# Kernel tuning notes

Hardware: AMD Instinct MI355X
Metric: run time of the kernel (lower is better)

## Reference

```python
import jax, jax.numpy as jnp
import numpy as np

AXES = 72        # NUM_OF_IMU_AXES
PARAMS = 12      # NUM_OF_NOISE_PARAMS
MAX_PROP = 600   # max_propogation
LN_EPS = 1e-5    # nn.LayerNorm default eps


def setup_inputs() -> dict:
    key = jax.random.key(0)
    k0, k1 = jax.random.split(key, 2)
    S, D = 4096, 512
    hidden_states = jax.random.normal(k0, (1, S, D), jnp.float32)
    gamma = jnp.ones((D,), jnp.float32)          # LayerNorm weight
    beta = jnp.zeros((D,), jnp.float32)          # LayerNorm bias
    W = jax.random.normal(k1, (D, AXES * PARAMS), jnp.float32) * 0.02  # Linear weight (in,out)
    b = jnp.zeros((AXES * PARAMS,), jnp.float32)
    return {"hidden_states": hidden_states, "gamma": gamma, "beta": beta, "W": W, "b": b}


def reference(hidden_states, gamma, beta, W, b):
    S = hidden_states.shape[1]
    T = min(MAX_PROP, S)  # time_steps_propogate_kinematics (static under jit)

    # LayerNorm over last dim
    x = hidden_states[0]  # (S, D); B == 1 by contract
    mu = jnp.mean(x, axis=-1, keepdims=True)
    var = jnp.mean((x - mu) ** 2, axis=-1, keepdims=True)
    xn = (x - mu) / jnp.sqrt(var + LN_EPS) * gamma + beta

    # Linear -> (seq, params, axes); rearrange 'seq (params axes)' => params outer
    p = (xn @ W + b).reshape(S, PARAMS, AXES)
    sp = jax.nn.softplus

    c, c_th = p[:, 4], p[:, 5]          # (S, A)
    phi, phi_th = p[:, 6], p[:, 7]
    d = sp(p[:, 1]); k = d * d / 4 + sp(p[:, 0])
    d_th = sp(p[:, 3]); k_th = d_th * d_th / 4 + sp(p[:, 2])

    acc_base = p[:, 8].T                # (A, S)
    acc_std = sp(p[:, 9]).T
    gyro_base = p[:, 10].T
    gyro_std = sp(p[:, 11]).T

    t = jnp.arange(T, dtype=jnp.float32)[None, :, None]  # (1, T, 1)

    def osc(cc, dd, kk, ph):
        # damped oscillator value grid, vectorized over all 72 axes: (S, T, A)
        om = jnp.sqrt(4.0 * kk - dd * dd) / 2.0  # = sqrt(softplus)>=0, safe
        return (cc[:, None, :] * jnp.exp(-dd[:, None, :] / 2.0 * t)
                * jnp.sin(t * om[:, None, :] + ph[:, None, :]))

    vals = osc(c, d, k, phi) + osc(c_th, d_th, k_th, phi_th)  # (S, T, A)

    # banded overlap-add: out[s + t] += vals[s, t]; positions >= S are dropped
    pos = (jnp.arange(S)[:, None] + jnp.arange(T)[None, :]).reshape(-1)  # (S*T,)
    vals_flat = vals.reshape(S * T, AXES)
    out = jnp.zeros((S + T, AXES), vals.dtype).at[pos].add(vals_flat)[:S]  # (S, A)
    kinematics = out.T  # (A, S)

    return kinematics, acc_base, acc_std, gyro_base, gyro_std
```

## Files before the change

### kernel.cpp

```cpp
#include <hip/hip_runtime.h>
#include <math.h>

#define S_TOTAL 4096
#define DDIM    512
#define AXES    72
#define NPROJ   864
#define T_PROP  600
#define SA      (S_TOTAL*AXES)
#define LN_EPS  1e-5f
#define AMP_CUT 4e-6f

typedef __attribute__((ext_vector_type(8))) short short8;
typedef __attribute__((ext_vector_type(4))) float f32x4;

__device__ __forceinline__ float softplus_f(float x) {
    return fmaxf(x, 0.f) + log1pf(expf(-fabsf(x)));
}
__device__ __forceinline__ unsigned short bf_hi(float f) {
    return (unsigned short)(__float_as_uint(f) >> 16);
}

__global__ __launch_bounds__(256) void prep_kernel(
        const float* __restrict__ x, const float* __restrict__ gamma,
        const float* __restrict__ beta, const float* __restrict__ W,
        unsigned short* __restrict__ Ahi, unsigned short* __restrict__ Alo,
        unsigned short* __restrict__ WhiT, unsigned short* __restrict__ WloT,
        float* __restrict__ kin) {
    __shared__ float Wt[32][33];
    int tid = threadIdx.x;
    int b = blockIdx.x;
    if (b < 1024) {
        int lane = tid & 63, w = tid >> 6;
        int row = b*4 + w;
        const float4* xr = reinterpret_cast<const float4*>(x + (size_t)row * DDIM);
        float4 xv[2] = { xr[lane], xr[lane + 64] };
        float sum = 0.f, ssq = 0.f;
#pragma unroll
        for (int c = 0; c < 2; ++c) {
            sum += (xv[c].x + xv[c].y) + (xv[c].z + xv[c].w);
            ssq += xv[c].x*xv[c].x + xv[c].y*xv[c].y + xv[c].z*xv[c].z + xv[c].w*xv[c].w;
        }
#pragma unroll
        for (int off = 1; off < 64; off <<= 1) {
            sum += __shfl_xor(sum, off);
            ssq += __shfl_xor(ssq, off);
        }
        float m = sum * (1.f/DDIM);
        float r = rsqrtf(ssq * (1.f/DDIM) - m*m + LN_EPS);
        const float4* gp = reinterpret_cast<const float4*>(gamma);
        const float4* bp = reinterpret_cast<const float4*>(beta);
#pragma unroll
        for (int c = 0; c < 2; ++c) {
            float4 gv = gp[lane + 64*c], bv = bp[lane + 64*c];
            float xn[4] = {(xv[c].x-m)*r*gv.x+bv.x, (xv[c].y-m)*r*gv.y+bv.y,
                           (xv[c].z-m)*r*gv.z+bv.z, (xv[c].w-m)*r*gv.w+bv.w};
            ushort4 h4, l4;
            unsigned short* hp = &h4.x;
            unsigned short* lp = &l4.x;
#pragma unroll
            for (int j = 0; j < 4; ++j) {
                unsigned short hi = bf_hi(xn[j]);
                float fhi = __uint_as_float((unsigned)hi << 16);
                hp[j] = hi;
                lp[j] = bf_hi(xn[j] - fhi);
            }
            size_t o = (size_t)row*DDIM + 256*c + lane*4;
            *reinterpret_cast<ushort4*>(&Ahi[o]) = h4;
            *reinterpret_cast<ushort4*>(&Alo[o]) = l4;
        }
    } else if (b < 1456) {
        int wb = b - 1024;
        int bk = wb / 27, bn = wb - bk*27;
        int tx = tid & 31, ty0 = tid >> 5;
#pragma unroll
        for (int rr = 0; rr < 4; ++rr) {
            int ty = ty0 + rr*8;
            Wt[ty][tx] = W[(size_t)(bk*32 + ty)*NPROJ + bn*32 + tx];
        }
        __syncthreads();
#pragma unroll
        for (int rr = 0; rr < 4; ++rr) {
            int ny = ty0 + rr*8;
            int n = bn*32 + ny;
            int k = bk*32 + tx;
            float f = Wt[tx][ny];
            unsigned short hi = bf_hi(f);
            float fhi = __uint_as_float((unsigned)hi << 16);
            WhiT[(size_t)n*DDIM + k] = hi;
            WloT[(size_t)n*DDIM + k] = bf_hi(f - fhi);
        }
    } else {
        int zb = b - 1456;
        float4 z4 = make_float4(0.f, 0.f, 0.f, 0.f);
        float4* kp = reinterpret_cast<float4*>(kin);
#pragma unroll
        for (int i = 0; i < 8; ++i)
            kp[zb*2048 + i*256 + tid] = z4;
    }
}

__global__ __launch_bounds__(256) void gemm_kernel(
        const unsigned short* __restrict__ Ahi, const unsigned short* __restrict__ Alo,
        const unsigned short* __restrict__ WhiT, const unsigned short* __restrict__ WloT,
        const float* __restrict__ bias,
        float* __restrict__ P, float* __restrict__ out) {
    __shared__ __align__(16) unsigned short ldsArena[2*20480];

    int tid  = threadIdx.x;
    int lane = tid & 63;
    int wv   = tid >> 6;
    int wm   = wv & 1;
    int wn   = wv >> 1;
    int sBase = blockIdx.x * 64;
    int nBase = blockIdx.y * 96;
    int l15 = lane & 15;
    int r7  = l15 & 7;

    int rr = lane >> 3;
    int jj = ((lane & 7) ^ rr) * 8;
    const unsigned short* gp[10];
#pragma unroll
    for (int g = 0; g < 10; ++g) {
        int seg = wv*10 + g;
        const unsigned short* src;
        int row;
        if (seg < 16) {
            int p = seg >> 3, rg = seg & 7;
            row = sBase + rg*8 + rr;
            src = p ? Alo : Ahi;
        } else {
            int s2 = seg - 16;
            int p = (s2 >= 12) ? 1 : 0, rg = s2 - p*12;
            row = nBase + rg*8 + rr;
            src = p ? WloT : WhiT;
        }
        gp[g] = src + (size_t)row*DDIM + jj;
    }

    f32x4 acc[2][3] = {};
    int cur = 0;

#define STAGE(buf, k0) do {                                                   \
        unsigned short* lb = ldsArena + (buf)*20480 + wv*5120;                \
        _Pragma("unroll")                                                     \
        for (int g = 0; g < 10; ++g)                                          \
            __builtin_amdgcn_global_load_lds(                                 \
                (const __attribute__((address_space(1))) void*)(gp[g] + (k0)),\
                (__attribute__((address_space(3))) void*)(lb + g*512),        \
                16, 0, 0);                                                    \
    } while (0)

    STAGE(0, 0);

#pragma unroll 1
    for (int kt = 0; kt < 8; ++kt) {
        __syncthreads();
        if (kt < 7) STAGE(cur ^ 1, (kt+1)*64);

        const char* Bc = (const char*)(ldsArena + cur*20480);
#pragma unroll
        for (int kk = 0; kk < 2; ++kk) {
            int kb = kk*64 + ((lane>>4)<<4);
            short8 xh[2], xl[2], wh[3], wl[3];
#pragma unroll
            for (int mi = 0; mi < 2; ++mi) {
                int row = wm*32 + mi*16 + l15;
                int ad = (row*128 + kb) ^ (r7<<4);
                xh[mi] = *reinterpret_cast<const short8*>(Bc + ad);
                xl[mi] = *reinterpret_cast<const short8*>(Bc + 8192 + ad);
            }
#pragma unroll
            for (int nf = 0; nf < 3; ++nf) {
                int row = wn*48 + nf*16 + l15;
                int ad = (row*128 + kb) ^ (r7<<4);
                wh[nf] = *reinterpret_cast<const short8*>(Bc + 16384 + ad);
                wl[nf] = *reinterpret_cast<const short8*>(Bc + 28672 + ad);
            }
#pragma unroll
            for (int mi = 0; mi < 2; ++mi)
#pragma unroll
                for (int nf = 0; nf < 3; ++nf)
                    acc[mi][nf] = __builtin_amdgcn_mfma_f32_16x16x32_bf16(wh[nf], xh[mi], acc[mi][nf], 0, 0, 0);
#pragma unroll
            for (int mi = 0; mi < 2; ++mi)
#pragma unroll
                for (int nf = 0; nf < 3; ++nf)
                    acc[mi][nf] = __builtin_amdgcn_mfma_f32_16x16x32_bf16(wh[nf], xl[mi], acc[mi][nf], 0, 0, 0);
#pragma unroll
            for (int mi = 0; mi < 2; ++mi)
#pragma unroll
                for (int nf = 0; nf < 3; ++nf)
                    acc[mi][nf] = __builtin_amdgcn_mfma_f32_16x16x32_bf16(wl[nf], xh[mi], acc[mi][nf], 0, 0, 0);
        }
        cur ^= 1;
    }
#undef STAGE

    int sCol = sBase + wm*32 + l15;
    int nRowBase = nBase + wn*48 + ((lane>>4)<<2);
#pragma unroll
    for (int mi = 0; mi < 2; ++mi) {
        int s = sCol + mi*16;
#pragma unroll
        for (int nf = 0; nf < 3; ++nf) {
#pragma unroll
            for (int r = 0; r < 4; ++r) {
                int n = nRowBase + nf*16 + r;
                float val = acc[mi][nf][r] + bias[n];
                int ip = (n * 3641) >> 18;
                int a  = n - ip * 72;
                float res;
                if (ip == 0 || ip == 2)      res = sqrtf(softplus_f(val));
                else if (ip == 1 || ip == 3 || ip == 9 || ip == 11) res = softplus_f(val);
                else                          res = val;
                float* dst = (ip < 8) ? (P + (size_t)ip * SA)
                                      : (out + (size_t)(ip - 7) * SA);
                dst[(size_t)a * S_TOTAL + s] = res;
            }
        }
    }
}

template<int STEPS>
__device__ __forceinline__ void osc_chunk(
        float& v1a, float& v1b, float& v2a, float& v2b,
        float p1, float q1, float p2, float q2,
        float& acc0, float& acc1, int lane, int lane4) {
#pragma unroll
    for (int i = 0; i < STEPS/2; ++i) {
        {
            const int dt = 2*i;
            v1b = fmaf(p1, v1a, -(q1*v1b));
            v2b = fmaf(p2, v2a, -(q2*v2b));
            float v = v1b + v2b;
            if (dt == 0) {
                acc0 += v;
            } else {
                int addr = (lane4 + (((64-dt)&63)<<2)) & 255;
                float vr = __int_as_float(__builtin_amdgcn_ds_bpermute(addr, __float_as_int(v)));
                bool nw = lane >= dt;
                acc0 += nw ? vr : 0.f;
                acc1 += nw ? 0.f : vr;
            }
        }
        {
            const int dt = 2*i + 1;
            v1a = fmaf(p1, v1b, -(q1*v1a));
            v2a = fmaf(p2, v2b, -(q2*v2a));
            float v = v1a + v2a;
            int addr = (lane4 + (((64-dt)&63)<<2)) & 255;
            float vr = __int_as_float(__builtin_amdgcn_ds_bpermute(addr, __float_as_int(v)));
            bool nw = lane >= dt;
            acc0 += nw ? vr : 0.f;
            acc1 += nw ? 0.f : vr;
        }
    }
}

__global__ __launch_bounds__(256) void osc_kernel(const float* __restrict__ P,
                                                  float* __restrict__ kin) {
    int tid  = threadIdx.x;
    int lane = tid & 63;
    int wv   = tid >> 6;
    int lane4 = lane << 2;
    int sBase = blockIdx.x * 64;
    int a  = blockIdx.y * 2 + (wv >> 1);
    int t0 = (wv & 1) * 300;
    float t0f = (float)t0;

    size_t base = (size_t)a * S_TOTAL + sBase + lane;
    float om1 = P[0*(size_t)SA + base], d1 = P[1*(size_t)SA + base];
    float om2 = P[2*(size_t)SA + base], d2 = P[3*(size_t)SA + base];
    float c1  = P[4*(size_t)SA + base], c2  = P[5*(size_t)SA + base];
    float ph1 = P[6*(size_t)SA + base], ph2 = P[7*(size_t)SA + base];

    float dcf1 = __expf(-0.5f*d1);
    float e1   = c1 * __expf(-0.5f*d1*t0f);
    float s0, c0, so, co;
    __sincosf(fmaf(t0f, om1, ph1), &s0, &c0);
    __sincosf(om1, &so, &co);
    float inv1 = __expf(0.5f*d1);
    float p1 = 2.f*dcf1*co, q1 = dcf1*dcf1;
    float v1a = e1*inv1*(s0*co - c0*so);
    float cs2 = fmaf(2.f*co, co, -1.f), sn2 = 2.f*so*co;
    float v1b = e1*inv1*inv1*(s0*cs2 - c0*sn2);
    float amp1 = fabsf(e1);
    float dq1 = q1*q1; dq1*=dq1; dq1*=dq1; dq1*=dq1; dq1*=dq1;
    float dcf2 = __expf(-0.5f*d2);
    float e2   = c2 * __expf(-0.5f*d2*t0f);
    __sincosf(fmaf(t0f, om2, ph2), &s0, &c0);
    __sincosf(om2, &so, &co);
    float inv2 = __expf(0.5f*d2);
    float p2 = 2.f*dcf2*co, q2 = dcf2*dcf2;
    float v2a = e2*inv2*(s0*co - c0*so);
    cs2 = fmaf(2.f*co, co, -1.f); sn2 = 2.f*so*co;
    float v2b = e2*inv2*inv2*(s0*cs2 - c0*sn2);
    float amp2 = fabsf(e2);
    float dq2 = q2*q2; dq2*=dq2; dq2*=dq2; dq2*=dq2; dq2*=dq2;

    float acc0 = 0.f, acc1 = 0.f;
    float* kinA = kin + (size_t)a * S_TOTAL;
    int jBase = sBase + t0;
    int ran = 0;

#pragma unroll 1
    for (int c = 0; c < 5; ++c) {
        if (__all(fmaxf(amp1, amp2) < AMP_CUT)) break;
        if (c < 4) osc_chunk<64>(v1a, v1b, v2a, v2b, p1, q1, p2, q2, acc0, acc1, lane, lane4);
        else       osc_chunk<44>(v1a, v1b, v2a, v2b, p1, q1, p2, q2, acc0, acc1, lane, lane4);
        int j = jBase + lane;
        if (j < S_TOTAL) unsafeAtomicAdd(&kinA[j], acc0);
        acc0 = acc1; acc1 = 0.f;
        jBase += 64;
        amp1 *= dq1; amp2 *= dq2;
        ran = 1;
        if (jBase >= S_TOTAL) { ran = 0; break; }
    }
    if (ran) {
        int j = jBase + lane;
        if (j < S_TOTAL) unsafeAtomicAdd(&kinA[j], acc0);
    }
}

extern "C" void kernel_launch(void* const* d_in, const int* in_sizes, int n_in,
                              void* d_out, int out_size, void* d_ws, size_t ws_size,
                              hipStream_t stream) {
    const float* x     = (const float*)d_in[0];
    const float* gamma = (const float*)d_in[1];
    const float* beta  = (const float*)d_in[2];
    const float* W     = (const float*)d_in[3];
    const float* b     = (const float*)d_in[4];
    float* out = (float*)d_out;

    unsigned char* wsb = (unsigned char*)d_ws;
    float* P    = (float*)wsb;
    unsigned short* Ahi  = (unsigned short*)(wsb + 9437184);
    unsigned short* Alo  = Ahi  + (size_t)S_TOTAL*DDIM;
    unsigned short* WhiT = Alo  + (size_t)S_TOTAL*DDIM;
    unsigned short* WloT = WhiT + (size_t)NPROJ*DDIM;

    prep_kernel<<<dim3(1024 + 432 + 36), dim3(256), 0, stream>>>(x, gamma, beta, W,
                                                                 Ahi, Alo, WhiT, WloT, out);
    gemm_kernel<<<dim3(S_TOTAL/64, NPROJ/96), dim3(256), 0, stream>>>(Ahi, Alo, WhiT, WloT,
                                                                      b, P, out);
    osc_kernel<<<dim3(S_TOTAL/64, AXES/2), dim3(256), 0, stream>>>(P, out);
}
```

Before: 61.15 us.

## Load GEMM operands directly from global memory, dropping LDS staging

Removes the double-buffered LDS staging (global_load_lds plus barriers) from the split-bf16 GEMM. Each lane now reads its 16-byte MFMA fragments straight from global memory. The grid is also transposed so that N-blocks sharing an S tile run next to each other, which is meant to improve L2 reuse of the activation rows. This trades away the barriers and LDS traffic for redundant global/L2 reads across waves, since each A tile is reread by both wn waves and each W tile by both wm waves, and the loads become less coalesced.

```diff
diff --git a/kernel.cpp b/kernel.cpp
--- a/kernel.cpp
+++ b/kernel.cpp
@@ -104,100 +104,66 @@
         const unsigned short* __restrict__ WhiT, const unsigned short* __restrict__ WloT,
         const float* __restrict__ bias,
         float* __restrict__ P, float* __restrict__ out) {
-    __shared__ __align__(16) unsigned short ldsArena[2*20480];
-
     int tid  = threadIdx.x;
     int lane = tid & 63;
     int wv   = tid >> 6;
     int wm   = wv & 1;
     int wn   = wv >> 1;
-    int sBase = blockIdx.x * 64;
-    int nBase = blockIdx.y * 96;
+    int nBase = blockIdx.x * 96;
+    int sBase = blockIdx.y * 64;
     int l15 = lane & 15;
-    int r7  = l15 & 7;
-
-    int rr = lane >> 3;
-    int jj = ((lane & 7) ^ rr) * 8;
-    const unsigned short* gp[10];
-#pragma unroll
-    for (int g = 0; g < 10; ++g) {
-        int seg = wv*10 + g;
-        const unsigned short* src;
-        int row;
-        if (seg < 16) {
-            int p = seg >> 3, rg = seg & 7;
-            row = sBase + rg*8 + rr;
-            src = p ? Alo : Ahi;
-        } else {
-            int s2 = seg - 16;
-            int p = (s2 >= 12) ? 1 : 0, rg = s2 - p*12;
-            row = nBase + rg*8 + rr;
-            src = p ? WloT : WhiT;
-        }
-        gp[g] = src + (size_t)row*DDIM + jj;
+    int g   = lane >> 4;
+
+    const short8* xb[2][2];
+    const short8* wb[2][3];
+#pragma unroll
+    for (int mi = 0; mi < 2; ++mi) {
+        size_t o = (size_t)(sBase + wm*32 + mi*16 + l15) * DDIM + g*8;
+        xb[0][mi] = reinterpret_cast<const short8*>(Ahi + o);
+        xb[1][mi] = reinterpret_cast<const short8*>(Alo + o);
+    }
+#pragma unroll
+    for (int nf = 0; nf < 3; ++nf) {
+        size_t o = (size_t)(nBase + wn*48 + nf*16 + l15) * DDIM + g*8;
+        wb[0][nf] = reinterpret_cast<const short8*>(WhiT + o);
+        wb[1][nf] = reinterpret_cast<const short8*>(WloT + o);
     }
 
     f32x4 acc[2][3] = {};
-    int cur = 0;
-
-#define STAGE(buf, k0) do {                                                   \
-        unsigned short* lb = ldsArena + (buf)*20480 + wv*5120;                \
-        _Pragma("unroll")                                                     \
-        for (int g = 0; g < 10; ++g)                                          \
-            __builtin_amdgcn_global_load_lds(                                 \
-                (const __attribute__((address_space(1))) void*)(gp[g] + (k0)),\
-                (__attribute__((address_space(3))) void*)(lb + g*512),        \
-                16, 0, 0);                                                    \
-    } while (0)
-
-    STAGE(0, 0);
-
-#pragma unroll 1
-    for (int kt = 0; kt < 8; ++kt) {
-        __syncthreads();
-        if (kt < 7) STAGE(cur ^ 1, (kt+1)*64);
-
-        const char* Bc = (const char*)(ldsArena + cur*20480);
-#pragma unroll
-        for (int kk = 0; kk < 2; ++kk) {
-            int kb = kk*64 + ((lane>>4)<<4);
-            short8 xh[2], xl[2], wh[3], wl[3];
-#pragma unroll
-            for (int mi = 0; mi < 2; ++mi) {
-                int row = wm*32 + mi*16 + l15;
-                int ad = (row*128 + kb) ^ (r7<<4);
-                xh[mi] = *reinterpret_cast<const short8*>(Bc + ad);
-                xl[mi] = *reinterpret_cast<const short8*>(Bc + 8192 + ad);
-            }
-#pragma unroll
-            for (int nf = 0; nf < 3; ++nf) {
-                int row = wn*48 + nf*16 + l15;
-                int ad = (row*128 + kb) ^ (r7<<4);
-                wh[nf] = *reinterpret_cast<const short8*>(Bc + 16384 + ad);
-                wl[nf] = *reinterpret_cast<const short8*>(Bc + 28672 + ad);
-            }
-#pragma unroll
-            for (int mi = 0; mi < 2; ++mi)
-#pragma unroll
-                for (int nf = 0; nf < 3; ++nf)
-                    acc[mi][nf] = __builtin_amdgcn_mfma_f32_16x16x32_bf16(wh[nf], xh[mi], acc[mi][nf], 0, 0, 0);
-#pragma unroll
-            for (int mi = 0; mi < 2; ++mi)
-#pragma unroll
-                for (int nf = 0; nf < 3; ++nf)
-                    acc[mi][nf] = __builtin_amdgcn_mfma_f32_16x16x32_bf16(wh[nf], xl[mi], acc[mi][nf], 0, 0, 0);
-#pragma unroll
-            for (int mi = 0; mi < 2; ++mi)
-#pragma unroll
-                for (int nf = 0; nf < 3; ++nf)
-                    acc[mi][nf] = __builtin_amdgcn_mfma_f32_16x16x32_bf16(wl[nf], xh[mi], acc[mi][nf], 0, 0, 0);
-        }
-        cur ^= 1;
-    }
-#undef STAGE
+
+#pragma unroll 2
+    for (int kt = 0; kt < 16; ++kt) {
+        int ko = kt * 4;
+        short8 xh[2], xl[2], wh[3], wl[3];
+#pragma unroll
+        for (int mi = 0; mi < 2; ++mi) {
+            xh[mi] = xb[0][mi][ko];
+            xl[mi] = xb[1][mi][ko];
+        }
+#pragma unroll
+        for (int nf = 0; nf < 3; ++nf) {
+            wh[nf] = wb[0][nf][ko];
+            wl[nf] = wb[1][nf][ko];
+        }
+#pragma unroll
+        for (int mi = 0; mi < 2; ++mi)
+#pragma unroll
+            for (int nf = 0; nf < 3; ++nf)
+                acc[mi][nf] = __builtin_amdgcn_mfma_f32_16x16x32_bf16(wh[nf], xh[mi], acc[mi][nf], 0, 0, 0);
+#pragma unroll
+        for (int mi = 0; mi < 2; ++mi)
+#pragma unroll
+            for (int nf = 0; nf < 3; ++nf)
+                acc[mi][nf] = __builtin_amdgcn_mfma_f32_16x16x32_bf16(wh[nf], xl[mi], acc[mi][nf], 0, 0, 0);
+#pragma unroll
+        for (int mi = 0; mi < 2; ++mi)
+#pragma unroll
+            for (int nf = 0; nf < 3; ++nf)
+                acc[mi][nf] = __builtin_amdgcn_mfma_f32_16x16x32_bf16(wl[nf], xh[mi], acc[mi][nf], 0, 0, 0);
+    }
 
     int sCol = sBase + wm*32 + l15;
-    int nRowBase = nBase + wn*48 + ((lane>>4)<<2);
+    int nRowBase = nBase + wn*48 + (g<<2);
 #pragma unroll
     for (int mi = 0; mi < 2; ++mi) {
         int s = sCol + mi*16;
@@ -341,7 +307,7 @@
 
     prep_kernel<<<dim3(1024 + 432 + 36), dim3(256), 0, stream>>>(x, gamma, beta, W,
                                                                  Ahi, Alo, WhiT, WloT, out);
-    gemm_kernel<<<dim3(S_TOTAL/64, NPROJ/96), dim3(256), 0, stream>>>(Ahi, Alo, WhiT, WloT,
+    gemm_kernel<<<dim3(NPROJ/96, S_TOTAL/64), dim3(256), 0, stream>>>(Ahi, Alo, WhiT, WloT,
                                                                       b, P, out);
     osc_kernel<<<dim3(S_TOTAL/64, AXES/2), dim3(256), 0, stream>>>(P, out);
 }
```

Result: slower. 100.8 us (+64.9%).

## Restructure GEMM K-loop into explicit two-buffer pipeline with fine-grained vmcnt waits

Applied to the files above, without the earlier changes.

The GEMM main loop is unrolled by two with statically indexed LDS buffers. Both stages are prefetched up front, and each compute phase waits only for its own buffer's async global-to-LDS loads using s_waitcnt vmcnt(10) instead of a full drain at __syncthreads. LDS addresses are also precomputed per row and k-half to cut address arithmetic. This aims to keep one buffer's loads in flight during compute, at the cost of an extra barrier per stage and reliance on exact vmcnt accounting.

```diff
diff --git a/kernel.cpp b/kernel.cpp
--- a/kernel.cpp
+++ b/kernel.cpp
@@ -114,14 +114,15 @@
     int sBase = blockIdx.x * 64;
     int nBase = blockIdx.y * 96;
     int l15 = lane & 15;
+    int g   = lane >> 4;
     int r7  = l15 & 7;
 
     int rr = lane >> 3;
     int jj = ((lane & 7) ^ rr) * 8;
     const unsigned short* gp[10];
 #pragma unroll
-    for (int g = 0; g < 10; ++g) {
-        int seg = wv*10 + g;
+    for (int sg = 0; sg < 10; ++sg) {
+        int seg = wv*10 + sg;
         const unsigned short* src;
         int row;
         if (seg < 16) {
@@ -134,70 +135,87 @@
             row = nBase + rg*8 + rr;
             src = p ? WloT : WhiT;
         }
-        gp[g] = src + (size_t)row*DDIM + jj;
-    }
+        gp[sg] = src + (size_t)row*DDIM + jj;
+    }
+
+    int koff0 = (g*16) ^ (r7<<4);
+    int koff1 = (64 + g*16) ^ (r7<<4);
+    int rowXb[2], rowWb[3];
+#pragma unroll
+    for (int mi = 0; mi < 2; ++mi) rowXb[mi] = (wm*32 + mi*16 + l15) * 128;
+#pragma unroll
+    for (int nf = 0; nf < 3; ++nf) rowWb[nf] = (wn*48 + nf*16 + l15) * 128;
 
     f32x4 acc[2][3] = {};
-    int cur = 0;
-
-#define STAGE(buf, k0) do {                                                   \
+
+#define STAGE(buf, kt) do {                                                   \
         unsigned short* lb = ldsArena + (buf)*20480 + wv*5120;                \
         _Pragma("unroll")                                                     \
-        for (int g = 0; g < 10; ++g)                                          \
+        for (int sg = 0; sg < 10; ++sg)                                       \
             __builtin_amdgcn_global_load_lds(                                 \
-                (const __attribute__((address_space(1))) void*)(gp[g] + (k0)),\
-                (__attribute__((address_space(3))) void*)(lb + g*512),        \
+                (const __attribute__((address_space(1))) void*)(gp[sg] + (kt)*64), \
+                (__attribute__((address_space(3))) void*)(lb + sg*512),       \
                 16, 0, 0);                                                    \
     } while (0)
 
+#define COMPUTE(BUF) do {                                                     \
+        const char* Bc = (const char*)ldsArena + (BUF)*40960;                 \
+        _Pragma("unroll")                                                     \
+        for (int kk = 0; kk < 2; ++kk) {                                      \
+            int ko = kk ? koff1 : koff0;                                      \
+            short8 xh[2], xl[2], wh[3], wl[3];                                \
+            _Pragma("unroll")                                                 \
+            for (int mi = 0; mi < 2; ++mi) {                                  \
+                xh[mi] = *reinterpret_cast<const short8*>(Bc + rowXb[mi] + ko);        \
+                xl[mi] = *reinterpret_cast<const short8*>(Bc + 8192 + rowXb[mi] + ko); \
+            }                                                                 \
+            _Pragma("unroll")                                                 \
+            for (int nf = 0; nf < 3; ++nf) {                                  \
+                wh[nf] = *reinterpret_cast<const short8*>(Bc + 16384 + rowWb[nf] + ko); \
+                wl[nf] = *reinterpret_cast<const short8*>(Bc + 28672 + rowWb[nf] + ko); \
+            }                                                                 \
+            _Pragma("unroll")                                                 \
+            for (int mi = 0; mi < 2; ++mi)                                    \
+                _Pragma("unroll")                                             \
+                for (int nf = 0; nf < 3; ++nf)                                \
+                    acc[mi][nf] = __builtin_amdgcn_mfma_f32_16x16x32_bf16(wh[nf], xh[mi], acc[mi][nf], 0, 0, 0); \
+            _Pragma("unroll")                                                 \
+            for (int mi = 0; mi < 2; ++mi)                                    \
+                _Pragma("unroll")                                             \
+                for (int nf = 0; nf < 3; ++nf)                                \
+                    acc[mi][nf] = __builtin_amdgcn_mfma_f32_16x16x32_bf16(wh[nf], xl[mi], acc[mi][nf], 0, 0, 0); \
+            _Pragma("unroll")                                                 \
+            for (int mi = 0; mi < 2; ++mi)                                    \
+                _Pragma("unroll")                                             \
+                for (int nf = 0; nf < 3; ++nf)                                \
+                    acc[mi][nf] = __builtin_amdgcn_mfma_f32_16x16x32_bf16(wl[nf], xh[mi], acc[mi][nf], 0, 0, 0); \
+        }                                                                     \
+    } while (0)
+
     STAGE(0, 0);
+    STAGE(1, 1);
 
 #pragma unroll 1
-    for (int kt = 0; kt < 8; ++kt) {
-        __syncthreads();
-        if (kt < 7) STAGE(cur ^ 1, (kt+1)*64);
-
-        const char* Bc = (const char*)(ldsArena + cur*20480);
-#pragma unroll
-        for (int kk = 0; kk < 2; ++kk) {
-            int kb = kk*64 + ((lane>>4)<<4);
-            short8 xh[2], xl[2], wh[3], wl[3];
-#pragma unroll
-            for (int mi = 0; mi < 2; ++mi) {
-                int row = wm*32 + mi*16 + l15;
-                int ad = (row*128 + kb) ^ (r7<<4);
-                xh[mi] = *reinterpret_cast<const short8*>(Bc + ad);
-                xl[mi] = *reinterpret_cast<const short8*>(Bc + 8192 + ad);
-            }
-#pragma unroll
-            for (int nf = 0; nf < 3; ++nf) {
-                int row = wn*48 + nf*16 + l15;
-                int ad = (row*128 + kb) ^ (r7<<4);
-                wh[nf] = *reinterpret_cast<const short8*>(Bc + 16384 + ad);
-                wl[nf] = *reinterpret_cast<const short8*>(Bc + 28672 + ad);
-            }
-#pragma unroll
-            for (int mi = 0; mi < 2; ++mi)
-#pragma unroll
-                for (int nf = 0; nf < 3; ++nf)
-                    acc[mi][nf] = __builtin_amdgcn_mfma_f32_16x16x32_bf16(wh[nf], xh[mi], acc[mi][nf], 0, 0, 0);
-#pragma unroll
-            for (int mi = 0; mi < 2; ++mi)
-#pragma unroll
-                for (int nf = 0; nf < 3; ++nf)
-                    acc[mi][nf] = __builtin_amdgcn_mfma_f32_16x16x32_bf16(wh[nf], xl[mi], acc[mi][nf], 0, 0, 0);
-#pragma unroll
-            for (int mi = 0; mi < 2; ++mi)
-#pragma unroll
-                for (int nf = 0; nf < 3; ++nf)
-                    acc[mi][nf] = __builtin_amdgcn_mfma_f32_16x16x32_bf16(wl[nf], xh[mi], acc[mi][nf], 0, 0, 0);
-        }
-        cur ^= 1;
+    for (int kt2 = 0; kt2 < 4; ++kt2) {
+        asm volatile("s_waitcnt vmcnt(10)" ::: "memory");
+        __builtin_amdgcn_sched_barrier(0);
+        __builtin_amdgcn_s_barrier();
+        COMPUTE(0);
+        __builtin_amdgcn_s_barrier();
+        if (kt2 < 3) STAGE(0, 2*kt2 + 2);
+        if (kt2 < 3) { asm volatile("s_waitcnt vmcnt(10)" ::: "memory"); }
+        else         { asm volatile("s_waitcnt vmcnt(0)"  ::: "memory"); }
+        __builtin_amdgcn_sched_barrier(0);
+        __builtin_amdgcn_s_barrier();
+        COMPUTE(1);
+        __builtin_amdgcn_s_barrier();
+        if (kt2 < 3) STAGE(1, 2*kt2 + 3);
     }
 #undef STAGE
+#undef COMPUTE
 
     int sCol = sBase + wm*32 + l15;
-    int nRowBase = nBase + wn*48 + ((lane>>4)<<2);
+    int nRowBase = nBase + wn*48 + (g<<2);
 #pragma unroll
     for (int mi = 0; mi < 2; ++mi) {
         int s = sCol + mi*16;
```

After: 64.47 us. 5.4% more time.
